# Kernel optimization log

Hardware: AMD Instinct MI355X
Metric: run time of the kernel (lower is better)

## Reference

```python
import jax, jax.numpy as jnp
import numpy as np

B, T = 32, 2048
Q_DIM, K_DIM, V_DIM, A_DIM = 512, 512, 512, 128
TEMP = 1.0


def setup_inputs() -> dict:
    key = jax.random.key(0)
    ks = jax.random.split(key, 8)
    return {
        "query": jax.random.normal(ks[0], (B, Q_DIM), dtype=jnp.float32),
        "keys": jax.random.normal(ks[1], (B, T, K_DIM), dtype=jnp.float32),
        "values": jax.random.normal(ks[2], (B, T, V_DIM), dtype=jnp.float32),
        "prev_attention_weights": jax.random.uniform(ks[3], (B, T), dtype=jnp.float32),
        "mask": jnp.ones((B, T), dtype=jnp.int32),
        # learned params (nn.Linear weight is [out,in]; store as [in,out])
        "Wq": jax.random.normal(ks[4], (Q_DIM, A_DIM), dtype=jnp.float32) * 0.02,
        "Wk": jax.random.normal(ks[5], (K_DIM, A_DIM), dtype=jnp.float32) * 0.02,
        "We": jax.random.normal(ks[6], (A_DIM, 1), dtype=jnp.float32) * 0.02,
    }


def reference(query, keys, values, prev_attention_weights, mask, Wq, Wk, We):
    # additive attention energies
    qp = query @ Wq                                   # [B, A]
    kp = jnp.einsum('btk,ka->bta', keys, Wk)          # [B, T, A]
    energy = jnp.squeeze(jnp.tanh(kp + qp[:, None, :]) @ We, -1)  # [B, T]
    energy = jnp.where(mask == 0, -jnp.inf, energy)
    raw = jax.nn.softmax(energy / TEMP, axis=1)
    # forward attention: fw[0]=raw[0]; fw[t]=(prev[t-1]+prev[t])*raw[t] for t>=1
    prev = prev_attention_weights
    prev_shift = jnp.pad(prev[:, :-1], ((0, 0), (1, 0)))  # prev[t-1], zero at t=0
    fw = raw * (prev + prev_shift)
    fw = fw.at[:, 0].set(raw[:, 0])
    fw = fw / (fw.sum(axis=1, keepdims=True) + 1e-8)
    context = jnp.einsum('bt,btd->bd', fw, values)    # [B, V_DIM]
    return context, fw
```

## Files before the change

### kernel.cpp

```cpp
#include <hip/hip_runtime.h>
#include <cstdint>
#include <cstddef>


#define T_ 2048
#define KD 512
#define AD 128

typedef __attribute__((ext_vector_type(8))) short bf16x8;
typedef __attribute__((ext_vector_type(4))) float f32x4;

__device__ __forceinline__ unsigned pack2bf(float a, float b) {
    unsigned ua = __float_as_uint(a), ub = __float_as_uint(b);
    ua += 0x7FFFu + ((ua >> 16) & 1u);
    ub += 0x7FFFu + ((ub >> 16) & 1u);
    return (ua >> 16) | (ub & 0xFFFF0000u);
}

__global__ __launch_bounds__(256) void prep_kernel(
    const float* __restrict__ query, const float* __restrict__ Wq,
    const float* __restrict__ Wk, float* __restrict__ qp,
    unsigned short* __restrict__ WkT)
{
    __shared__ float sq[128];
    const int tid = threadIdx.x;
    if (blockIdx.x < 32) {
        const int b = blockIdx.x;
        const int a = tid & 127, half = tid >> 7;
        const float* q = query + (size_t)b * KD + half * 256;
        const float* w = Wq + (size_t)(half * 256) * AD + a;
        float s0 = 0.f, s1 = 0.f, s2 = 0.f, s3 = 0.f;
        #pragma unroll 4
        for (int k = 0; k < 256; k += 4) {
            s0 += q[k + 0] * w[(size_t)(k + 0) * AD];
            s1 += q[k + 1] * w[(size_t)(k + 1) * AD];
            s2 += q[k + 2] * w[(size_t)(k + 2) * AD];
            s3 += q[k + 3] * w[(size_t)(k + 3) * AD];
        }
        float s = (s0 + s1) + (s2 + s3);
        if (half == 0) sq[a] = s;
        __syncthreads();
        if (half == 1) qp[(size_t)b * AD + a] = sq[a] + s;
    } else {
        const int blk2 = blockIdx.x - 32;
        const int n = tid & 127, kr = tid >> 7;
        #pragma unroll
        for (int kk = 0; kk < 8; kk++) {
            int k = blk2 * 16 + kr * 8 + kk;
            float v = Wk[(size_t)k * AD + n];
            unsigned u = __float_as_uint(v);
            u += 0x7FFFu + ((u >> 16) & 1u);
            WkT[(size_t)n * KD + k] = (unsigned short)(u >> 16);
        }
    }
}

__global__ __launch_bounds__(256, 2) void energy_kernel(
    const float* __restrict__ keys, const unsigned short* __restrict__ WkT,
    const float* __restrict__ qp, const float* __restrict__ We,
    float* __restrict__ energy)
{
    __shared__ __align__(16) unsigned short sA[128 * 40];
    __shared__ __align__(16) unsigned short sB[128 * 40];
    const int tid = threadIdx.x;
    const int m0 = blockIdx.x * 128;
    const int b = m0 >> 11;

    const int row = tid >> 1, half = tid & 1;
    const float* gA = keys + (size_t)(m0 + row) * KD + half * 16;
    const unsigned short* gB = WkT + (size_t)row * KD + half * 16;
    unsigned short* dA = &sA[row * 40 + half * 16];
    unsigned short* dB = &sB[row * 40 + half * 16];

    const int lane = tid & 63, wv = tid >> 6;
    const int lr = lane & 15, quad = lane >> 4;

    f32x4 acc[2][8];
    #pragma unroll
    for (int mt = 0; mt < 2; mt++)
        #pragma unroll
        for (int nt = 0; nt < 8; nt++)
            acc[mt][nt] = (f32x4){0.f, 0.f, 0.f, 0.f};

    for (int k0 = 0; k0 < KD; k0 += 32) {
        float4 f0 = *(const float4*)(gA + k0 + 0);
        float4 f1 = *(const float4*)(gA + k0 + 4);
        float4 f2 = *(const float4*)(gA + k0 + 8);
        float4 f3 = *(const float4*)(gA + k0 + 12);
        uint4 pa0, pa1;
        pa0.x = pack2bf(f0.x, f0.y); pa0.y = pack2bf(f0.z, f0.w);
        pa0.z = pack2bf(f1.x, f1.y); pa0.w = pack2bf(f1.z, f1.w);
        pa1.x = pack2bf(f2.x, f2.y); pa1.y = pack2bf(f2.z, f2.w);
        pa1.z = pack2bf(f3.x, f3.y); pa1.w = pack2bf(f3.z, f3.w);
        uint4 b0 = *(const uint4*)(gB + k0);
        uint4 b1 = *(const uint4*)(gB + k0 + 8);
        ((uint4*)dA)[0] = pa0; ((uint4*)dA)[1] = pa1;
        ((uint4*)dB)[0] = b0;  ((uint4*)dB)[1] = b1;
        __syncthreads();

        bf16x8 af[2], bfm[8];
        #pragma unroll
        for (int mt = 0; mt < 2; mt++)
            af[mt] = *(const bf16x8*)&sA[(wv * 32 + mt * 16 + lr) * 40 + quad * 8];
        #pragma unroll
        for (int nt = 0; nt < 8; nt++)
            bfm[nt] = *(const bf16x8*)&sB[(nt * 16 + lr) * 40 + quad * 8];
        #pragma unroll
        for (int mt = 0; mt < 2; mt++)
            #pragma unroll
            for (int nt = 0; nt < 8; nt++)
                acc[mt][nt] = __builtin_amdgcn_mfma_f32_16x16x32_bf16(
                    af[mt], bfm[nt], acc[mt][nt], 0, 0, 0);
        __syncthreads();
    }

    float part[2][4] = {{0.f, 0.f, 0.f, 0.f}, {0.f, 0.f, 0.f, 0.f}};
    #pragma unroll
    for (int nt = 0; nt < 8; nt++) {
        int col = nt * 16 + lr;
        float we = We[col];
        float q  = qp[(size_t)b * AD + col];
        #pragma unroll
        for (int mt = 0; mt < 2; mt++)
            #pragma unroll
            for (int r = 0; r < 4; r++) {
                float x = acc[mt][nt][r] + q;
                float e2 = __expf(2.0f * x);
                float th = 1.0f - 2.0f / (e2 + 1.0f);
                part[mt][r] += we * th;
            }
    }
    #pragma unroll
    for (int mt = 0; mt < 2; mt++)
        #pragma unroll
        for (int r = 0; r < 4; r++) {
            float v = part[mt][r];
            v += __shfl_xor(v, 1); v += __shfl_xor(v, 2);
            v += __shfl_xor(v, 4); v += __shfl_xor(v, 8);
            if (lr == 0)
                energy[(size_t)m0 + wv * 32 + mt * 16 + quad * 4 + r] = v;
        }
}

__device__ __forceinline__ float block_red_max(float v, float* sred) {
    #pragma unroll
    for (int m = 1; m < 64; m <<= 1) v = fmaxf(v, __shfl_xor(v, m));
    if ((threadIdx.x & 63) == 0) sred[threadIdx.x >> 6] = v;
    __syncthreads();
    float r = fmaxf(fmaxf(sred[0], sred[1]), fmaxf(sred[2], sred[3]));
    __syncthreads();
    return r;
}
__device__ __forceinline__ float block_red_sum(float v, float* sred) {
    #pragma unroll
    for (int m = 1; m < 64; m <<= 1) v += __shfl_xor(v, m);
    if ((threadIdx.x & 63) == 0) sred[threadIdx.x >> 6] = v;
    __syncthreads();
    float r = (sred[0] + sred[1]) + (sred[2] + sred[3]);
    __syncthreads();
    return r;
}

__global__ __launch_bounds__(256) void softmax_fw_kernel(
    const float* __restrict__ prev, const int* __restrict__ mask,
    float* __restrict__ fw)
{
    __shared__ float sred[4];
    const int b = blockIdx.x, tid = threadIdx.x;
    const size_t base = (size_t)b * T_;
    float e[8];
    #pragma unroll
    for (int i = 0; i < 8; i++) {
        int t = tid + 256 * i;
        float ev = fw[base + t];
        if (mask[base + t] == 0) ev = -__builtin_inff();
        e[i] = ev;
    }
    float mx = e[0];
    #pragma unroll
    for (int i = 1; i < 8; i++) mx = fmaxf(mx, e[i]);
    mx = block_red_max(mx, sred);

    float ex[8]; float s = 0.f;
    #pragma unroll
    for (int i = 0; i < 8; i++) { ex[i] = __expf(e[i] - mx); s += ex[i]; }
    s = block_red_sum(s, sred);
    const float invS = 1.0f / s;

    float fwv[8]; float s2 = 0.f;
    #pragma unroll
    for (int i = 0; i < 8; i++) {
        int t = tid + 256 * i;
        float pv = prev[base + t];
        float pm = (t == 0) ? 0.f : prev[base + t - 1];
        float r = ex[i] * invS;
        fwv[i] = (t == 0) ? r : r * (pv + pm);
        s2 += fwv[i];
    }
    s2 = block_red_sum(s2, sred);
    const float invD = 1.0f / (s2 + 1e-8f);
    #pragma unroll
    for (int i = 0; i < 8; i++)
        fw[base + tid + 256 * i] = fwv[i] * invD;
}

__global__ __launch_bounds__(256) void ctx_partial_kernel(
    const float* __restrict__ values, const float* __restrict__ fw,
    float* __restrict__ part)
{
    __shared__ float sfw[128];
    __shared__ float4 sacc[128];
    const int b = blockIdx.x >> 4, ts = blockIdx.x & 15;
    const int tid = threadIdx.x;
    const int t0 = ts * 128;
    if (tid < 128) sfw[tid] = fw[(size_t)b * T_ + t0 + tid];
    __syncthreads();
    const int d4 = tid & 127, tp = tid >> 7;
    const float4* vp = (const float4*)values + ((size_t)b * T_ + t0 + tp) * 128 + d4;
    float4 acc = {0.f, 0.f, 0.f, 0.f};
    #pragma unroll 4
    for (int i = 0; i < 64; i++) {
        float f = sfw[tp + 2 * i];
        float4 v = vp[(size_t)i * 256];
        acc.x += f * v.x; acc.y += f * v.y; acc.z += f * v.z; acc.w += f * v.w;
    }
    if (tp) sacc[d4] = acc;
    __syncthreads();
    if (!tp) {
        float4 o = sacc[d4];
        o.x += acc.x; o.y += acc.y; o.z += acc.z; o.w += acc.w;
        ((float4*)part)[(size_t)blockIdx.x * 128 + d4] = o;
    }
}

__global__ __launch_bounds__(256) void ctx_reduce_kernel(
    const float* __restrict__ part, float* __restrict__ ctx)
{
    const int idx = blockIdx.x * 256 + threadIdx.x;
    const int b = idx >> 9, d = idx & 511;
    float s = 0.f;
    #pragma unroll
    for (int ts = 0; ts < 16; ts++)
        s += part[((size_t)(b * 16 + ts)) * 512 + d];
    ctx[idx] = s;
}

extern "C" void kernel_launch(void* const* d_in, const int* in_sizes, int n_in,
                              void* d_out, int out_size, void* d_ws, size_t ws_size,
                              hipStream_t stream) {
    const float* query  = (const float*)d_in[0];
    const float* keys   = (const float*)d_in[1];
    const float* values = (const float*)d_in[2];
    const float* prev   = (const float*)d_in[3];
    const int*   mask   = (const int*)d_in[4];
    const float* Wq     = (const float*)d_in[5];
    const float* Wk     = (const float*)d_in[6];
    const float* We     = (const float*)d_in[7];

    float* ctx = (float*)d_out;
    float* fw  = ctx + 32 * 512;

    float* wsf = (float*)d_ws;
    float* qp   = wsf;
    float* part = wsf + 4096;
    unsigned short* WkT = (unsigned short*)(wsf + 4096 + 262144);

    prep_kernel<<<dim3(64), dim3(256), 0, stream>>>(query, Wq, Wk, qp, WkT);
    energy_kernel<<<dim3(512), dim3(256), 0, stream>>>(keys, WkT, qp, We, fw);
    softmax_fw_kernel<<<dim3(32), dim3(256), 0, stream>>>(prev, mask, fw);
    ctx_partial_kernel<<<dim3(512), dim3(256), 0, stream>>>(values, fw, part);
    ctx_reduce_kernel<<<dim3(64), dim3(256), 0, stream>>>(part, ctx);
}
```

Baseline: 310.8 us.

## Load MFMA operands directly from global, widen softmax blocks, split context finer

The energy GEMM no longer stages keys and WkT through LDS with per-tile barriers. Each lane now loads its MFMA fragments straight from global memory, using nontemporal loads for keys, and processes 64 K per iteration. The softmax kernel moves to 1024 threads per row, and the context partial kernel splits T into 32 chunks with nontemporal value loads, which doubles the partial buffer and the reduce length. The aim is to remove LDS and sync overhead and raise memory parallelism. The cost is uncoalesced, redundant WkT reads across waves and more partial traffic.

New measurement: 318.7 us. +2.6%, slower.

```diff
diff --git a/kernel.cpp b/kernel.cpp
--- a/kernel.cpp
+++ b/kernel.cpp
@@ -15,6 +15,10 @@
     ua += 0x7FFFu + ((ua >> 16) & 1u);
     ub += 0x7FFFu + ((ub >> 16) & 1u);
     return (ua >> 16) | (ub & 0xFFFF0000u);
+}
+
+__device__ __forceinline__ f32x4 ntld4(const float* p) {
+    return __builtin_nontemporal_load((const f32x4*)p);
 }
 
 __global__ __launch_bounds__(256) void prep_kernel(
@@ -60,20 +64,15 @@
     const float* __restrict__ qp, const float* __restrict__ We,
     float* __restrict__ energy)
 {
-    __shared__ __align__(16) unsigned short sA[128 * 40];
-    __shared__ __align__(16) unsigned short sB[128 * 40];
     const int tid = threadIdx.x;
+    const int lane = tid & 63, wv = tid >> 6;
+    const int lr = lane & 15, quad = lane >> 4;
     const int m0 = blockIdx.x * 128;
     const int b = m0 >> 11;
 
-    const int row = tid >> 1, half = tid & 1;
-    const float* gA = keys + (size_t)(m0 + row) * KD + half * 16;
-    const unsigned short* gB = WkT + (size_t)row * KD + half * 16;
-    unsigned short* dA = &sA[row * 40 + half * 16];
-    unsigned short* dB = &sB[row * 40 + half * 16];
-
-    const int lane = tid & 63, wv = tid >> 6;
-    const int lr = lane & 15, quad = lane >> 4;
+    const float* a0 = keys + (size_t)(m0 + wv * 32 + lr) * KD + quad * 8;
+    const float* a1 = a0 + (size_t)16 * KD;
+    const unsigned short* bp = WkT + (size_t)lr * KD + quad * 8;
 
     f32x4 acc[2][8];
     #pragma unroll
@@ -82,36 +81,39 @@
         for (int nt = 0; nt < 8; nt++)
             acc[mt][nt] = (f32x4){0.f, 0.f, 0.f, 0.f};
 
-    for (int k0 = 0; k0 < KD; k0 += 32) {
-        float4 f0 = *(const float4*)(gA + k0 + 0);
-        float4 f1 = *(const float4*)(gA + k0 + 4);
-        float4 f2 = *(const float4*)(gA + k0 + 8);
-        float4 f3 = *(const float4*)(gA + k0 + 12);
-        uint4 pa0, pa1;
-        pa0.x = pack2bf(f0.x, f0.y); pa0.y = pack2bf(f0.z, f0.w);
-        pa0.z = pack2bf(f1.x, f1.y); pa0.w = pack2bf(f1.z, f1.w);
-        pa1.x = pack2bf(f2.x, f2.y); pa1.y = pack2bf(f2.z, f2.w);
-        pa1.z = pack2bf(f3.x, f3.y); pa1.w = pack2bf(f3.z, f3.w);
-        uint4 b0 = *(const uint4*)(gB + k0);
-        uint4 b1 = *(const uint4*)(gB + k0 + 8);
-        ((uint4*)dA)[0] = pa0; ((uint4*)dA)[1] = pa1;
-        ((uint4*)dB)[0] = b0;  ((uint4*)dB)[1] = b1;
-        __syncthreads();
-
-        bf16x8 af[2], bfm[8];
-        #pragma unroll
-        for (int mt = 0; mt < 2; mt++)
-            af[mt] = *(const bf16x8*)&sA[(wv * 32 + mt * 16 + lr) * 40 + quad * 8];
-        #pragma unroll
-        for (int nt = 0; nt < 8; nt++)
-            bfm[nt] = *(const bf16x8*)&sB[(nt * 16 + lr) * 40 + quad * 8];
-        #pragma unroll
-        for (int mt = 0; mt < 2; mt++)
+    for (int k0 = 0; k0 < KD; k0 += 64) {
+        f32x4 fa[2][4];
+        bf16x8 bfr[2][8];
+        #pragma unroll
+        for (int h = 0; h < 2; h++) {
+            const int kk = k0 + h * 32;
+            fa[h][0] = ntld4(a0 + kk);
+            fa[h][1] = ntld4(a0 + kk + 4);
+            fa[h][2] = ntld4(a1 + kk);
+            fa[h][3] = ntld4(a1 + kk + 4);
             #pragma unroll
             for (int nt = 0; nt < 8; nt++)
-                acc[mt][nt] = __builtin_amdgcn_mfma_f32_16x16x32_bf16(
-                    af[mt], bfm[nt], acc[mt][nt], 0, 0, 0);
-        __syncthreads();
+                bfr[h][nt] = *(const bf16x8*)(bp + (size_t)nt * 16 * KD + kk);
+        }
+        #pragma unroll
+        for (int h = 0; h < 2; h++) {
+            union { bf16x8 v; unsigned u[4]; } A0, A1;
+            A0.u[0] = pack2bf(fa[h][0].x, fa[h][0].y);
+            A0.u[1] = pack2bf(fa[h][0].z, fa[h][0].w);
+            A0.u[2] = pack2bf(fa[h][1].x, fa[h][1].y);
+            A0.u[3] = pack2bf(fa[h][1].z, fa[h][1].w);
+            A1.u[0] = pack2bf(fa[h][2].x, fa[h][2].y);
+            A1.u[1] = pack2bf(fa[h][2].z, fa[h][2].w);
+            A1.u[2] = pack2bf(fa[h][3].x, fa[h][3].y);
+            A1.u[3] = pack2bf(fa[h][3].z, fa[h][3].w);
+            #pragma unroll
+            for (int nt = 0; nt < 8; nt++) {
+                acc[0][nt] = __builtin_amdgcn_mfma_f32_16x16x32_bf16(
+                    A0.v, bfr[h][nt], acc[0][nt], 0, 0, 0);
+                acc[1][nt] = __builtin_amdgcn_mfma_f32_16x16x32_bf16(
+                    A1.v, bfr[h][nt], acc[1][nt], 0, 0, 0);
+            }
+        }
     }
 
     float part[2][4] = {{0.f, 0.f, 0.f, 0.f}, {0.f, 0.f, 0.f, 0.f}};
@@ -142,94 +144,94 @@
         }
 }
 
-__device__ __forceinline__ float block_red_max(float v, float* sred) {
+__device__ __forceinline__ float blk_max16(float v, float* sred) {
     #pragma unroll
     for (int m = 1; m < 64; m <<= 1) v = fmaxf(v, __shfl_xor(v, m));
     if ((threadIdx.x & 63) == 0) sred[threadIdx.x >> 6] = v;
     __syncthreads();
-    float r = fmaxf(fmaxf(sred[0], sred[1]), fmaxf(sred[2], sred[3]));
+    float r = sred[0];
+    #pragma unroll
+    for (int i = 1; i < 16; i++) r = fmaxf(r, sred[i]);
     __syncthreads();
     return r;
 }
-__device__ __forceinline__ float block_red_sum(float v, float* sred) {
+__device__ __forceinline__ float blk_sum16(float v, float* sred) {
     #pragma unroll
     for (int m = 1; m < 64; m <<= 1) v += __shfl_xor(v, m);
     if ((threadIdx.x & 63) == 0) sred[threadIdx.x >> 6] = v;
     __syncthreads();
-    float r = (sred[0] + sred[1]) + (sred[2] + sred[3]);
+    float r = 0.f;
+    #pragma unroll
+    for (int i = 0; i < 16; i++) r += sred[i];
     __syncthreads();
     return r;
 }
 
-__global__ __launch_bounds__(256) void softmax_fw_kernel(
+__global__ __launch_bounds__(1024) void softmax_fw_kernel(
     const float* __restrict__ prev, const int* __restrict__ mask,
     float* __restrict__ fw)
 {
-    __shared__ float sred[4];
+    __shared__ float sred[16];
     const int b = blockIdx.x, tid = threadIdx.x;
     const size_t base = (size_t)b * T_;
-    float e[8];
-    #pragma unroll
-    for (int i = 0; i < 8; i++) {
-        int t = tid + 256 * i;
+    float e[2];
+    #pragma unroll
+    for (int i = 0; i < 2; i++) {
+        int t = tid + 1024 * i;
         float ev = fw[base + t];
         if (mask[base + t] == 0) ev = -__builtin_inff();
         e[i] = ev;
     }
-    float mx = e[0];
-    #pragma unroll
-    for (int i = 1; i < 8; i++) mx = fmaxf(mx, e[i]);
-    mx = block_red_max(mx, sred);
-
-    float ex[8]; float s = 0.f;
-    #pragma unroll
-    for (int i = 0; i < 8; i++) { ex[i] = __expf(e[i] - mx); s += ex[i]; }
-    s = block_red_sum(s, sred);
+    float mx = blk_max16(fmaxf(e[0], e[1]), sred);
+
+    float ex[2];
+    ex[0] = __expf(e[0] - mx); ex[1] = __expf(e[1] - mx);
+    float s = blk_sum16(ex[0] + ex[1], sred);
     const float invS = 1.0f / s;
 
-    float fwv[8]; float s2 = 0.f;
-    #pragma unroll
-    for (int i = 0; i < 8; i++) {
-        int t = tid + 256 * i;
+    float fwv[2]; float s2 = 0.f;
+    #pragma unroll
+    for (int i = 0; i < 2; i++) {
+        int t = tid + 1024 * i;
         float pv = prev[base + t];
         float pm = (t == 0) ? 0.f : prev[base + t - 1];
         float r = ex[i] * invS;
         fwv[i] = (t == 0) ? r : r * (pv + pm);
         s2 += fwv[i];
     }
-    s2 = block_red_sum(s2, sred);
+    s2 = blk_sum16(s2, sred);
     const float invD = 1.0f / (s2 + 1e-8f);
     #pragma unroll
-    for (int i = 0; i < 8; i++)
-        fw[base + tid + 256 * i] = fwv[i] * invD;
+    for (int i = 0; i < 2; i++)
+        fw[base + tid + 1024 * i] = fwv[i] * invD;
 }
 
 __global__ __launch_bounds__(256) void ctx_partial_kernel(
     const float* __restrict__ values, const float* __restrict__ fw,
     float* __restrict__ part)
 {
-    __shared__ float sfw[128];
-    __shared__ float4 sacc[128];
-    const int b = blockIdx.x >> 4, ts = blockIdx.x & 15;
+    __shared__ float sfw[64];
+    __shared__ f32x4 sacc[128];
+    const int b = blockIdx.x >> 5, ts = blockIdx.x & 31;
     const int tid = threadIdx.x;
-    const int t0 = ts * 128;
-    if (tid < 128) sfw[tid] = fw[(size_t)b * T_ + t0 + tid];
+    const int t0 = ts * 64;
+    if (tid < 64) sfw[tid] = fw[(size_t)b * T_ + t0 + tid];
     __syncthreads();
     const int d4 = tid & 127, tp = tid >> 7;
-    const float4* vp = (const float4*)values + ((size_t)b * T_ + t0 + tp) * 128 + d4;
-    float4 acc = {0.f, 0.f, 0.f, 0.f};
-    #pragma unroll 4
-    for (int i = 0; i < 64; i++) {
+    const f32x4* vp = (const f32x4*)values + ((size_t)b * T_ + t0 + tp) * 128 + d4;
+    f32x4 acc = {0.f, 0.f, 0.f, 0.f};
+    #pragma unroll 16
+    for (int i = 0; i < 32; i++) {
         float f = sfw[tp + 2 * i];
-        float4 v = vp[(size_t)i * 256];
+        f32x4 v = __builtin_nontemporal_load(vp + (size_t)i * 256);
         acc.x += f * v.x; acc.y += f * v.y; acc.z += f * v.z; acc.w += f * v.w;
     }
     if (tp) sacc[d4] = acc;
     __syncthreads();
     if (!tp) {
-        float4 o = sacc[d4];
+        f32x4 o = sacc[d4];
         o.x += acc.x; o.y += acc.y; o.z += acc.z; o.w += acc.w;
-        ((float4*)part)[(size_t)blockIdx.x * 128 + d4] = o;
+        ((f32x4*)part)[(size_t)blockIdx.x * 128 + d4] = o;
     }
 }
 
@@ -240,8 +242,8 @@
     const int b = idx >> 9, d = idx & 511;
     float s = 0.f;
     #pragma unroll
-    for (int ts = 0; ts < 16; ts++)
-        s += part[((size_t)(b * 16 + ts)) * 512 + d];
+    for (int ts = 0; ts < 32; ts++)
+        s += part[((size_t)(b * 32 + ts)) * 512 + d];
     ctx[idx] = s;
 }
 
@@ -263,11 +265,11 @@
     float* wsf = (float*)d_ws;
     float* qp   = wsf;
     float* part = wsf + 4096;
-    unsigned short* WkT = (unsigned short*)(wsf + 4096 + 262144);
+    unsigned short* WkT = (unsigned short*)(wsf + 4096 + 524288);
 
     prep_kernel<<<dim3(64), dim3(256), 0, stream>>>(query, Wq, Wk, qp, WkT);
     energy_kernel<<<dim3(512), dim3(256), 0, stream>>>(keys, WkT, qp, We, fw);
-    softmax_fw_kernel<<<dim3(32), dim3(256), 0, stream>>>(prev, mask, fw);
-    ctx_partial_kernel<<<dim3(512), dim3(256), 0, stream>>>(values, fw, part);
+    softmax_fw_kernel<<<dim3(32), dim3(1024), 0, stream>>>(prev, mask, fw);
+    ctx_partial_kernel<<<dim3(1024), dim3(256), 0, stream>>>(values, fw, part);
     ctx_reduce_kernel<<<dim3(64), dim3(256), 0, stream>>>(part, ctx);
 }
```
